# Performance work log

Measured on AMD Instinct MI355X. Metric: run time of the kernel, lower is better.

Reference implementation:

```python
import jax, jax.numpy as jnp
import numpy as np

N = 256
BIG = 1e9  # acts as +inf for float32 duals


def solve_lap(C):
    """Exact linear assignment (min-cost) via Jonker-Volgenant shortest
    augmenting paths with dual potentials. Returns [n,n] 0/1 labelling with
    exactly one 1 per row and per column (same optimum as scipy's
    linear_sum_assignment, up to ties)."""
    n = C.shape[0]
    dt = C.dtype
    big = jnp.asarray(BIG, dt)
    # 1-indexed padded cost: row/col 0 are dummies
    C1 = jnp.zeros((n + 1, n + 1), dt).at[1:, 1:].set(C)

    def row_body(i, carry):
        u, v, p = carry  # u: row duals, v: col duals, p[j] = row matched to col j (0 = free)
        p = p.at[0].set(i)

        def cond(st):
            u, v, p, used, minv, way, j0 = st
            return p[j0] != 0

        def body(st):
            u, v, p, used, minv, way, j0 = st
            used = used.at[j0].set(True)
            i0 = p[j0]
            cur = C1[i0] - u[i0] - v            # reduced costs of row i0, all cols
            upd = (~used) & (cur < minv)
            minv = jnp.where(upd, cur, minv)
            way = jnp.where(upd, j0, way)
            masked = jnp.where(used, big, minv)
            j1 = jnp.argmin(masked).astype(jnp.int32)
            delta = masked[j1]
            u = u.at[p].add(jnp.where(used, delta, jnp.asarray(0, dt)))
            v = v - jnp.where(used, delta, jnp.asarray(0, dt))
            minv = minv - jnp.where(used, jnp.asarray(0, dt), delta)
            return (u, v, p, used, minv, way, j1)

        used0 = jnp.zeros(n + 1, bool)
        minv0 = jnp.full(n + 1, big, dt)
        way0 = jnp.zeros(n + 1, jnp.int32)
        u, v, p, used, minv, way, j0 = jax.lax.while_loop(
            cond, body, (u, v, p, used0, minv0, way0, jnp.int32(0)))

        # augment along the alternating path back to the dummy column 0
        def acond(st):
            p_, j = st
            return j != 0

        def abody(st):
            p_, j = st
            j1 = way[j]
            p_ = p_.at[j].set(p_[j1])
            return (p_, j1)

        p, _ = jax.lax.while_loop(acond, abody, (p, j0))
        return (u, v, p)

    u0 = jnp.zeros(n + 1, dt)
    v0 = jnp.zeros(n + 1, dt)
    p0 = jnp.zeros(n + 1, jnp.int32)
    u, v, p = jax.lax.fori_loop(1, n + 1, row_body, (u0, v0, p0))

    rows = p[1:] - 1                      # row matched to each col (0-based)
    cols = jnp.arange(n)
    return jnp.zeros((n, n), dt).at[rows, cols].set(jnp.asarray(1.0, dt))


def setup_inputs() -> dict:
    key = jax.random.key(0)
    unaries = jax.random.normal(key, (N, N), dtype=jnp.float32)
    return {"unaries": unaries}


def reference(unaries):
    # LAPSolverModule.forward: exact min-cost assignment -> 0/1 labelling matrix
    return solve_lap(unaries)
```

## Files before the change

### kernel.cpp

```cpp
#include <hip/hip_runtime.h>

#define NN 256
#define BIGF 1e9f
#define NROWS_LDS 152
#define SMEM_BYTES (NROWS_LDS * 256 * 4)
#define LDS_LIMIT (NROWS_LDS * 1024)

template <int CTRL>
__device__ __forceinline__ float dpp_fmin(float x) {
    int t = __builtin_amdgcn_update_dpp(__float_as_int(x), __float_as_int(x),
                                        CTRL, 0xf, 0xf, false);
    return fminf(x, __int_as_float(t));
}

__device__ __forceinline__ float wave_min_bcast(float x) {
    x = dpp_fmin<0x111>(x);
    x = dpp_fmin<0x112>(x);
    x = dpp_fmin<0x114>(x);
    x = dpp_fmin<0x118>(x);
    x = dpp_fmin<0x142>(x);
    x = dpp_fmin<0x143>(x);
    return __int_as_float(__builtin_amdgcn_readlane(__float_as_int(x), 63));
}

extern "C" __global__ __launch_bounds__(64)
void lap_solve(const float* __restrict__ C, float* __restrict__ out) {
    extern __shared__ float rowc[];
    const int lane = threadIdx.x;
    const int base = lane * 4;
    const int boff = base * 4 - 1024;

    {
        const float4* src = (const float4*)C;
        float4*       dst = (float4*)rowc;
        #pragma unroll 8
        for (int idx = lane; idx < NROWS_LDS * 64; idx += 64) dst[idx] = src[idx];
    }
    __syncthreads();

    float v0 = 0.f, v1 = 0.f, v2 = 0.f, v3 = 0.f;
    float a0 = 0.f, a1 = 0.f, a2 = 0.f, a3 = 0.f;
    int   p0 = 0,  p1 = 0,  p2 = 0,  p3 = 0;

    float4 r = *(const float4*)((const char*)rowc + ((1 << 10) + boff));

    for (int i = 1; i <= NN; ++i) {
        float m0 = BIGF, m1 = BIGF, m2 = BIGF, m3 = BIGF;
        int   w0 = 0, w1 = 0, w2 = 0, w3 = 0;
        int   q0 = 0, q1 = 0, q2 = 0, q3 = 0;
        float ui = 0.0f;
        float u0 = 0.0f;
        int   j0 = 0, jF = 0;

        for (int guard = 0; guard < 300; ++guard) {
            float c0 = (r.x - u0) - v0;
            float c1 = (r.y - u0) - v1;
            float c2 = (r.z - u0) - v2;
            float c3 = (r.w - u0) - v3;
            if (!q0 && c0 < m0) { m0 = c0; w0 = j0; }
            if (!q1 && c1 < m1) { m1 = c1; w1 = j0; }
            if (!q2 && c2 < m2) { m2 = c2; w2 = j0; }
            if (!q3 && c3 < m3) { m3 = c3; w3 = j0; }

            float bv = fminf(fminf(m0, m1), fminf(m2, m3));
            int   bk = (m0 == bv) ? 0 : (m1 == bv) ? 1 : (m2 == bv) ? 2 : 3;
            int   rc = (bk == 0) ? p0 : (bk == 1) ? p1 : (bk == 2) ? p2 : p3;
            float ra = (bk == 0) ? a0 : (bk == 1) ? a1 : (bk == 2) ? a2 : a3;
            int   packed = (rc << 10) | (base + bk + 1);

            float gmin = wave_min_bcast(bv);
            unsigned long long bal = __ballot(bv == gmin);
            int wl = (int)__builtin_ctzll(bal | 0x8000000000000000ULL);

            int rdl    = __builtin_amdgcn_readlane(packed, wl);
            int rowoff = rdl & ~1023;
            int j1     = rdl & 1023;

            float4 rn;
            if (rowoff <= LDS_LIMIT)
                rn = *(const float4*)((const char*)rowc + (rowoff + boff));
            else
                rn = *(const float4*)((const char*)C + (rowoff + boff));

            float u0n = __int_as_float(__builtin_amdgcn_readlane(__float_as_int(ra), wl));

            float delta = gmin;
            if (q0) { a0 += delta; v0 -= delta; }
            if (q1) { a1 += delta; v1 -= delta; }
            if (q2) { a2 += delta; v2 -= delta; }
            if (q3) { a3 += delta; v3 -= delta; }
            m0 -= delta;
            m1 -= delta;
            m2 -= delta;
            m3 -= delta;
            ui += delta;

            if (lane == wl) {
                if (bk == 0)      { q0 = 1; m0 = BIGF; }
                else if (bk == 1) { q1 = 1; m1 = BIGF; }
                else if (bk == 2) { q2 = 1; m2 = BIGF; }
                else              { q3 = 1; m3 = BIGF; }
            }

            j0 = j1; u0 = u0n; r = rn;
            if (rowoff == 0) { jF = j1; break; }
        }

        {
            int ni = (i < NN) ? (i + 1) : NN;
            int off = (ni << 10) + boff;
            if (ni <= NROWS_LDS) r = *(const float4*)((const char*)rowc + off);
            else                 r = *(const float4*)((const char*)C + off);
        }

        int j = jF;
        for (int g2w = 0; g2w < 300 && j != 0; ++g2w) {
            int oj = (j - 1) >> 2, sj = (j - 1) & 3;
            int wsel = (sj == 0) ? w0 : (sj == 1) ? w1 : (sj == 2) ? w2 : w3;
            int jn = __builtin_amdgcn_readlane(wsel, oj);
            int pn; float an;
            if (jn == 0) { pn = i; an = ui; }
            else {
                int on = (jn - 1) >> 2, sn = (jn - 1) & 3;
                int   ps = (sn == 0) ? p0 : (sn == 1) ? p1 : (sn == 2) ? p2 : p3;
                float as = (sn == 0) ? a0 : (sn == 1) ? a1 : (sn == 2) ? a2 : a3;
                pn = __builtin_amdgcn_readlane(ps, on);
                an = __int_as_float(__builtin_amdgcn_readlane(__float_as_int(as), on));
            }
            if (lane == oj) {
                if (sj == 0)      { p0 = pn; a0 = an; }
                else if (sj == 1) { p1 = pn; a1 = an; }
                else if (sj == 2) { p2 = pn; a2 = an; }
                else              { p3 = pn; a3 = an; }
            }
            j = jn;
        }
    }

    if (p0) out[(p0 - 1) * NN + base + 0] = 1.0f;
    if (p1) out[(p1 - 1) * NN + base + 1] = 1.0f;
    if (p2) out[(p2 - 1) * NN + base + 2] = 1.0f;
    if (p3) out[(p3 - 1) * NN + base + 3] = 1.0f;
}

extern "C" void kernel_launch(void* const* d_in, const int* in_sizes, int n_in,
                              void* d_out, int out_size, void* d_ws, size_t ws_size,
                              hipStream_t stream) {
    const float* C   = (const float*)d_in[0];
    float*       out = (float*)d_out;

    static_assert(SMEM_BYTES <= 160 * 1024, "LDS budget");
    (void)hipFuncSetAttribute((const void*)lap_solve,
                              hipFuncAttributeMaxDynamicSharedMemorySize,
                              SMEM_BYTES);

    (void)hipMemsetAsync(out, 0, NN * NN * sizeof(float), stream);
    lap_solve<<<dim3(1), dim3(64), SMEM_BYTES, stream>>>(C, out);
}
```

Measured before the change: 1.014 ms.

## Use packed f32 math and SGPR ballot masks for the LAP inner loop

Reworks the per-step update of the single-wave Hungarian solver. Column duals, row potentials and minima are held as float2 pairs and updated with v_pk_add_f32. The per-column 'used' flags become scalar wave masks, so conditional updates use v_cndmask with SGPR masks instead of divergent branches. The argmin winner and its column slot are found with per-slot ballots instead of a packed readlane of a per-lane index. This shortens the serial dependency chain of each augmenting-path step, but adds extra ballots and scalar bit logic on that same path.

```diff
diff --git a/kernel.cpp b/kernel.cpp
--- a/kernel.cpp
+++ b/kernel.cpp
@@ -5,6 +5,8 @@
 #define NROWS_LDS 152
 #define SMEM_BYTES (NROWS_LDS * 256 * 4)
 #define LDS_LIMIT (NROWS_LDS * 1024)
+
+typedef float v2f __attribute__((ext_vector_type(2)));
 
 template <int CTRL>
 __device__ __forceinline__ float dpp_fmin(float x) {
@@ -23,6 +25,32 @@
     return __int_as_float(__builtin_amdgcn_readlane(__float_as_int(x), 63));
 }
 
+__device__ __forceinline__ v2f pk_add(v2f a, v2f b) {
+    v2f d;
+    asm("v_pk_add_f32 %0, %1, %2" : "=v"(d) : "v"(a), "v"(b));
+    return d;
+}
+__device__ __forceinline__ v2f pk_sub(v2f a, v2f b) {
+    v2f d;
+    asm("v_pk_add_f32 %0, %1, %2 neg_lo:[0,1] neg_hi:[0,1]" : "=v"(d) : "v"(a), "v"(b));
+    return d;
+}
+__device__ __forceinline__ float sel0f(float tv, unsigned long long m) {
+    float d;
+    asm("v_cndmask_b32 %0, 0, %1, %2" : "=v"(d) : "v"(tv), "s"(m));
+    return d;
+}
+__device__ __forceinline__ float self_(float fv, float tv, unsigned long long m) {
+    float d;
+    asm("v_cndmask_b32 %0, %1, %2, %3" : "=v"(d) : "v"(fv), "v"(tv), "s"(m));
+    return d;
+}
+__device__ __forceinline__ int seli_(int fv, int tv, unsigned long long m) {
+    int d;
+    asm("v_cndmask_b32 %0, %1, %2, %3" : "=v"(d) : "v"(fv), "v"(tv), "s"(m));
+    return d;
+}
+
 extern "C" __global__ __launch_bounds__(64)
 void lap_solve(const float* __restrict__ C, float* __restrict__ out) {
     extern __shared__ float rowc[];
@@ -38,69 +66,79 @@
     }
     __syncthreads();
 
-    float v0 = 0.f, v1 = 0.f, v2 = 0.f, v3 = 0.f;
-    float a0 = 0.f, a1 = 0.f, a2 = 0.f, a3 = 0.f;
-    int   p0 = 0,  p1 = 0,  p2 = 0,  p3 = 0;
+    v2f V01 = {0.f, 0.f}, V23 = {0.f, 0.f};
+    v2f A01 = {0.f, 0.f}, A23 = {0.f, 0.f};
+    int p0 = 0, p1 = 0, p2 = 0, p3 = 0;
+    float vBIG = BIGF;
 
     float4 r = *(const float4*)((const char*)rowc + ((1 << 10) + boff));
 
     for (int i = 1; i <= NN; ++i) {
-        float m0 = BIGF, m1 = BIGF, m2 = BIGF, m3 = BIGF;
-        int   w0 = 0, w1 = 0, w2 = 0, w3 = 0;
-        int   q0 = 0, q1 = 0, q2 = 0, q3 = 0;
+        v2f M01 = {BIGF, BIGF}, M23 = {BIGF, BIGF};
+        int w0 = 0, w1 = 0, w2 = 0, w3 = 0;
+        unsigned long long Q0 = 0, Q1 = 0, Q2 = 0, Q3 = 0;
         float ui = 0.0f;
         float u0 = 0.0f;
         int   j0 = 0, jF = 0;
 
         for (int guard = 0; guard < 300; ++guard) {
-            float c0 = (r.x - u0) - v0;
-            float c1 = (r.y - u0) - v1;
-            float c2 = (r.z - u0) - v2;
-            float c3 = (r.w - u0) - v3;
-            if (!q0 && c0 < m0) { m0 = c0; w0 = j0; }
-            if (!q1 && c1 < m1) { m1 = c1; w1 = j0; }
-            if (!q2 && c2 < m2) { m2 = c2; w2 = j0; }
-            if (!q3 && c3 < m3) { m3 = c3; w3 = j0; }
+            v2f R01 = {r.x, r.y}, R23 = {r.z, r.w};
+            v2f U = {u0, u0};
+            v2f C01 = pk_sub(pk_sub(R01, U), V01);
+            v2f C23 = pk_sub(pk_sub(R23, U), V23);
 
-            float bv = fminf(fminf(m0, m1), fminf(m2, m3));
-            int   bk = (m0 == bv) ? 0 : (m1 == bv) ? 1 : (m2 == bv) ? 2 : 3;
-            int   rc = (bk == 0) ? p0 : (bk == 1) ? p1 : (bk == 2) ? p2 : p3;
-            float ra = (bk == 0) ? a0 : (bk == 1) ? a1 : (bk == 2) ? a2 : a3;
-            int   packed = (rc << 10) | (base + bk + 1);
+            unsigned long long cc0 = __ballot(C01.x < M01.x) & ~Q0;
+            unsigned long long cc1 = __ballot(C01.y < M01.y) & ~Q1;
+            unsigned long long cc2 = __ballot(C23.x < M23.x) & ~Q2;
+            unsigned long long cc3 = __ballot(C23.y < M23.y) & ~Q3;
+            int j0v;
+            asm("v_mov_b32 %0, %1" : "=v"(j0v) : "s"(j0));
+            M01.x = self_(M01.x, C01.x, cc0);  w0 = seli_(w0, j0v, cc0);
+            M01.y = self_(M01.y, C01.y, cc1);  w1 = seli_(w1, j0v, cc1);
+            M23.x = self_(M23.x, C23.x, cc2);  w2 = seli_(w2, j0v, cc2);
+            M23.y = self_(M23.y, C23.y, cc3);  w3 = seli_(w3, j0v, cc3);
 
+            float bv = fminf(fminf(M01.x, M01.y), fminf(M23.x, M23.y));
             float gmin = wave_min_bcast(bv);
-            unsigned long long bal = __ballot(bv == gmin);
-            int wl = (int)__builtin_ctzll(bal | 0x8000000000000000ULL);
 
-            int rdl    = __builtin_amdgcn_readlane(packed, wl);
-            int rowoff = rdl & ~1023;
-            int j1     = rdl & 1023;
+            unsigned long long b0 = __ballot(M01.x == gmin);
+            unsigned long long b1 = __ballot(M01.y == gmin);
+            unsigned long long b2 = __ballot(M23.x == gmin);
+            unsigned long long b3 = __ballot(M23.y == gmin);
+            unsigned long long anyb = b0 | b1 | b2 | b3;
+            int wl = (int)__builtin_ctzll(anyb | 0x8000000000000000ULL);
+            int sj = ((b0 >> wl) & 1) ? 0 : ((b1 >> wl) & 1) ? 1
+                   : ((b2 >> wl) & 1) ? 2 : 3;
+            int j1 = (wl << 2) + sj + 1;
 
+            int   psel = (sj == 0) ? p0 : (sj == 1) ? p1 : (sj == 2) ? p2 : p3;
+            int   pw   = __builtin_amdgcn_readlane(psel, wl);
+            int   rowoff = pw << 10;
             float4 rn;
             if (rowoff <= LDS_LIMIT)
                 rn = *(const float4*)((const char*)rowc + (rowoff + boff));
             else
                 rn = *(const float4*)((const char*)C + (rowoff + boff));
 
-            float u0n = __int_as_float(__builtin_amdgcn_readlane(__float_as_int(ra), wl));
+            float asel = (sj == 0) ? A01.x : (sj == 1) ? A01.y : (sj == 2) ? A23.x : A23.y;
+            float u0n  = __int_as_float(__builtin_amdgcn_readlane(__float_as_int(asel), wl));
 
             float delta = gmin;
-            if (q0) { a0 += delta; v0 -= delta; }
-            if (q1) { a1 += delta; v1 -= delta; }
-            if (q2) { a2 += delta; v2 -= delta; }
-            if (q3) { a3 += delta; v3 -= delta; }
-            m0 -= delta;
-            m1 -= delta;
-            m2 -= delta;
-            m3 -= delta;
+            float dv;
+            asm("v_mov_b32 %0, %1" : "=v"(dv) : "s"(delta));
+            v2f D01 = {sel0f(dv, Q0), sel0f(dv, Q1)};
+            v2f D23 = {sel0f(dv, Q2), sel0f(dv, Q3)};
+            A01 = pk_add(A01, D01);  V01 = pk_sub(V01, D01);
+            A23 = pk_add(A23, D23);  V23 = pk_sub(V23, D23);
+            v2f dd = {dv, dv};
+            M01 = pk_sub(M01, dd);   M23 = pk_sub(M23, dd);
             ui += delta;
 
-            if (lane == wl) {
-                if (bk == 0)      { q0 = 1; m0 = BIGF; }
-                else if (bk == 1) { q1 = 1; m1 = BIGF; }
-                else if (bk == 2) { q2 = 1; m2 = BIGF; }
-                else              { q3 = 1; m3 = BIGF; }
-            }
+            unsigned long long bit = 1ull << wl;
+            if (sj == 0)      { Q0 |= bit; M01.x = self_(M01.x, vBIG, bit); }
+            else if (sj == 1) { Q1 |= bit; M01.y = self_(M01.y, vBIG, bit); }
+            else if (sj == 2) { Q2 |= bit; M23.x = self_(M23.x, vBIG, bit); }
+            else              { Q3 |= bit; M23.y = self_(M23.y, vBIG, bit); }
 
             j0 = j1; u0 = u0n; r = rn;
             if (rowoff == 0) { jF = j1; break; }
@@ -115,23 +153,24 @@
 
         int j = jF;
         for (int g2w = 0; g2w < 300 && j != 0; ++g2w) {
-            int oj = (j - 1) >> 2, sj = (j - 1) & 3;
-            int wsel = (sj == 0) ? w0 : (sj == 1) ? w1 : (sj == 2) ? w2 : w3;
+            int oj = (j - 1) >> 2, sj2 = (j - 1) & 3;
+            int wsel = (sj2 == 0) ? w0 : (sj2 == 1) ? w1 : (sj2 == 2) ? w2 : w3;
             int jn = __builtin_amdgcn_readlane(wsel, oj);
             int pn; float an;
             if (jn == 0) { pn = i; an = ui; }
             else {
                 int on = (jn - 1) >> 2, sn = (jn - 1) & 3;
                 int   ps = (sn == 0) ? p0 : (sn == 1) ? p1 : (sn == 2) ? p2 : p3;
-                float as = (sn == 0) ? a0 : (sn == 1) ? a1 : (sn == 2) ? a2 : a3;
+                float as = (sn == 0) ? A01.x : (sn == 1) ? A01.y
+                         : (sn == 2) ? A23.x : A23.y;
                 pn = __builtin_amdgcn_readlane(ps, on);
                 an = __int_as_float(__builtin_amdgcn_readlane(__float_as_int(as), on));
             }
             if (lane == oj) {
-                if (sj == 0)      { p0 = pn; a0 = an; }
-                else if (sj == 1) { p1 = pn; a1 = an; }
-                else if (sj == 2) { p2 = pn; a2 = an; }
-                else              { p3 = pn; a3 = an; }
+                if (sj2 == 0)      { p0 = pn; A01.x = an; }
+                else if (sj2 == 1) { p1 = pn; A01.y = an; }
+                else if (sj2 == 2) { p2 = pn; A23.x = an; }
+                else               { p3 = pn; A23.y = an; }
             }
             j = jn;
         }
```

Measured after the change: 1.087 ms. +7.2%, slower.
